# Kernel optimization log

Hardware: AMD Instinct MI355X
Metric: run time of the kernel (lower is better)

## Reference

```python
import jax, jax.numpy as jnp
import numpy as np

CHANNELS = 256
HEADS = 8
HEAD_DIM = CHANNELS // HEADS
SCALE = HEAD_DIM ** (-0.5)


def setup_inputs() -> dict:
    key = jax.random.key(0)
    ks = jax.random.split(key, 9)
    x = jax.random.normal(ks[0], (2, CHANNELS, 64, 64), dtype=jnp.float32)
    # grouped 1x1 conv with groups=heads == per-head [head_dim, head_dim] matmul
    def w(k):
        # kaiming-uniform-ish init scale, faithful enough for a numeric baseline
        bound = 1.0 / np.sqrt(HEAD_DIM)
        return jax.random.uniform(k, (HEADS, HEAD_DIM, HEAD_DIM), dtype=jnp.float32,
                                  minval=-bound, maxval=bound)
    def b(k):
        bound = 1.0 / np.sqrt(HEAD_DIM)
        return jax.random.uniform(k, (HEADS, HEAD_DIM), dtype=jnp.float32,
                                  minval=-bound, maxval=bound)
    return {
        "x": x,
        "Wq": w(ks[1]), "bq": b(ks[2]),
        "Wk": w(ks[3]), "bk": b(ks[4]),
        "Wv": w(ks[5]), "bv": b(ks[6]),
        "Wp": w(ks[7]), "bp": b(ks[8]),
    }


def reference(x, Wq, bq, Wk, bk, Wv, bv, Wp, bp):
    b_, c, h, w = x.shape
    n = h * w
    xh = x.reshape(b_, HEADS, HEAD_DIM, n)  # [b, g, d, n]
    # grouped 1x1 conv == per-head linear over channel dim
    proj = lambda W, bias, t: jnp.einsum('god,bgdn->bgon', W, t) + bias[None, :, :, None]
    q = proj(Wq, bq, xh)  # [b, g, d, n]
    k = proj(Wk, bk, xh)
    v = proj(Wv, bv, xh)
    # attn[b,g,i,j] = sum_d q[b,g,d,i] * k[b,g,d,j] * scale
    attn = jnp.einsum('bgdi,bgdj->bgij', q, k) * SCALE
    attn = jax.nn.softmax(attn, axis=-1)  # [b, g, n, n]
    out = jnp.einsum('bgij,bgdj->bgdi', attn, v)  # [b, g, d, n]
    out = proj(Wp, bp, out)
    return out.reshape(b_, c, h, w)
```

## Files before the change

kernel.cpp:

```cpp
#include <hip/hip_runtime.h>
#include <hip/hip_bf16.h>


constexpr int D = 32;
constexpr int N = 4096;
constexpr int NBG = 16;
constexpr float SCALE = 0.17677669529663687f;
constexpr float LOG2E = 1.4426950408889634f;

using bfrag  = __attribute__((ext_vector_type(8))) short;
using s16x8  = __attribute__((ext_vector_type(8))) short;
using f32x16 = __attribute__((ext_vector_type(16))) float;
typedef unsigned short u16;
typedef unsigned int u32;

constexpr int PSTR = 34;

__device__ __forceinline__ float fexp2(float x) { return __builtin_amdgcn_exp2f(x); }

__device__ __forceinline__ short f2bfs(float f) {
    __hip_bfloat16 h = __float2bfloat16(f);
    return (short)__builtin_bit_cast(u16, h);
}

__device__ __forceinline__ u32 cvt_pk_bf16(float lo, float hi) {
    u32 r;
    asm("v_cvt_pk_bf16_f32 %0, %1, %2" : "=v"(r) : "v"(lo), "v"(hi));
    return r;
}

__global__ __launch_bounds__(256) void proj_kernel(
    const float* __restrict__ x,
    const float* __restrict__ Wq, const float* __restrict__ bq,
    const float* __restrict__ Wk, const float* __restrict__ bk,
    const float* __restrict__ Wv, const float* __restrict__ bv,
    u16* __restrict__ Qb, u16* __restrict__ K2, u16* __restrict__ V2) {
    const int bg = blockIdx.y, g = bg & 7;
    const int z  = blockIdx.z;
    const int i  = blockIdx.x * 256 + threadIdx.x;

    const float* W  = (z == 0) ? Wq : (z == 1) ? Wk : Wv;
    const float* bb = (z == 0) ? bq : (z == 1) ? bk : bv;

    const float* xb = x + (size_t)bg * D * N;
    float xv[D];
#pragma unroll
    for (int d = 0; d < D; ++d) xv[d] = xb[(size_t)d * N + i];

    const float* w = W + g * D * D;
    float acc[D];
#pragma unroll
    for (int o = 0; o < D; ++o) {
        float a0 = 0.f, a1 = 0.f, a2 = 0.f, a3 = 0.f;
#pragma unroll
        for (int d = 0; d < D; d += 4) {
            a0 = fmaf(w[o * D + d    ], xv[d    ], a0);
            a1 = fmaf(w[o * D + d + 1], xv[d + 1], a1);
            a2 = fmaf(w[o * D + d + 2], xv[d + 2], a2);
            a3 = fmaf(w[o * D + d + 3], xv[d + 3], a3);
        }
        acc[o] = (a0 + a1) + (a2 + a3) + bb[g * D + o];
    }

    if (z == 0) {
        u16* dst = Qb + ((size_t)bg * N + i) * D;
#pragma unroll
        for (int t = 0; t < 4; ++t) {
            s16x8 v;
#pragma unroll
            for (int e = 0; e < 8; ++e) v[e] = f2bfs(acc[8 * t + e] * (SCALE * LOG2E));
            *reinterpret_cast<s16x8*>(dst + 8 * t) = v;
        }
    } else if (z == 1) {
        u16* kb2 = K2 + (size_t)bg * N * D;
#pragma unroll
        for (int t = 0; t < 4; ++t) {
            s16x8 v;
#pragma unroll
            for (int e = 0; e < 8; ++e) v[e] = f2bfs(acc[8 * t + e]);
            *reinterpret_cast<s16x8*>(kb2 + (size_t)t * N * 8 + (size_t)i * 8) = v;
        }
    } else {
        const int j  = i & 15;
        const int hh = (j >> 2) & 1;
        const int ee = (j & 3) + 4 * ((j >> 3) & 1);
        u16* vb2 = V2 + (size_t)bg * N * D + (size_t)(i >> 4) * 512 + hh * 256 + ee;
#pragma unroll
        for (int o = 0; o < D; ++o)
            vb2[o * 8] = (u16)f2bfs(acc[o]);
    }
}

__global__ __launch_bounds__(256) void attn_kernel(
    const u16* __restrict__ Qb, const u16* __restrict__ K2, const u16* __restrict__ V2,
    const float* __restrict__ Wp, const float* __restrict__ bp,
    float* __restrict__ out) {
    const int s = blockIdx.x;
    const int bg = s & 15, qt = s >> 4, g = bg & 7;
    const int wid = threadIdx.x >> 6;
    const int lane = threadIdx.x & 63;
    const int l31 = lane & 31, h = lane >> 5;
    const int qbase = qt * 128 + wid * 32;

    __shared__ u16 plds_all[4][32][PSTR];
    u16* tile = &plds_all[wid][0][0];

    const u16* Qw = Qb + (size_t)bg * N * D;
    const u16* Kw = K2 + (size_t)bg * N * D;
    const u16* Vw = V2 + (size_t)bg * N * D;

    const u16* qrow = Qw + (size_t)(qbase + l31) * D + 8 * h;
    bfrag qf0 = *reinterpret_cast<const bfrag*>(qrow);
    bfrag qf1 = *reinterpret_cast<const bfrag*>(qrow + 16);

    bfrag wf0, wf1;
    {
        const float* wrow = Wp + (size_t)(g * D + l31) * D + 8 * h;
#pragma unroll
        for (int e = 0; e < 8; ++e) { wf0[e] = f2bfs(wrow[e]); wf1[e] = f2bfs(wrow[16 + e]); }
    }
    const float bias = bp[g * D + l31];

    bfrag onesf;
#pragma unroll
    for (int e = 0; e < 8; ++e) onesf[e] = (short)0x3F80;

    const f32x16 zf16 = {};
    f32x16 oacc  = {};
    f32x16 lsacc = {};

    const u16* kBase   = Kw + (size_t)h * N * 8 + (size_t)l31 * 8;
    const u16* kHiBase = kBase + 2 * N * 8;
    const u16* vBase   = Vw + h * 256 + l31 * 8;

    const int NT = N / 32;
    const int NP = NT / 2;

    auto ldK  = [&](int tt, int hi) {
        return *reinterpret_cast<const bfrag*>((hi ? kHiBase : kBase) + (size_t)tt * 256);
    };
    auto ldV  = [&](int tt, int half) {
        return *reinterpret_cast<const bfrag*>(vBase + (size_t)tt * 1024 + half * 512);
    };

    bfrag kA0 = ldK(0, 0), kA1 = ldK(0, 1);
    bfrag kB0 = ldK(1, 0), kB1 = ldK(1, 1);
    bfrag vA0 = ldV(0, 0), vA1 = ldV(0, 1);
    bfrag vB0 = ldV(1, 0), vB1 = ldV(1, 1);

    f32x16 sA = __builtin_amdgcn_mfma_f32_32x32x16_bf16(kA0, qf0, zf16, 0, 0, 0);
    sA = __builtin_amdgcn_mfma_f32_32x32x16_bf16(kA1, qf1, sA, 0, 0, 0);
    f32x16 sB = __builtin_amdgcn_mfma_f32_32x32x16_bf16(kB0, qf0, zf16, 0, 0, 0);
    sB = __builtin_amdgcn_mfma_f32_32x32x16_bf16(kB1, qf1, sB, 0, 0, 0);

    kA0 = ldK(2, 0); kA1 = ldK(2, 1);
    kB0 = ldK(3, 0); kB1 = ldK(3, 1);

    for (int t = 0; t < NP - 1; ++t) {
        f32x16 snA = __builtin_amdgcn_mfma_f32_32x32x16_bf16(kA0, qf0, zf16, 0, 0, 0);
        snA = __builtin_amdgcn_mfma_f32_32x32x16_bf16(kA1, qf1, snA, 0, 0, 0);
        f32x16 snB = __builtin_amdgcn_mfma_f32_32x32x16_bf16(kB0, qf0, zf16, 0, 0, 0);
        snB = __builtin_amdgcn_mfma_f32_32x32x16_bf16(kB1, qf1, snB, 0, 0, 0);

        const int t4 = (2 * t + 4 < NT) ? (2 * t + 4) : (NT - 1);
        const int t5 = (2 * t + 5 < NT) ? (2 * t + 5) : (NT - 1);
        kA0 = ldK(t4, 0); kA1 = ldK(t4, 1);
        kB0 = ldK(t5, 0); kB1 = ldK(t5, 1);
        bfrag vnA0 = ldV(2 * t + 2, 0), vnA1 = ldV(2 * t + 2, 1);
        bfrag vnB0 = ldV(2 * t + 3, 0), vnB1 = ldV(2 * t + 3, 1);

        {
            float p[16];
#pragma unroll
            for (int r = 0; r < 16; ++r) p[r] = fexp2(sA[r]);
            uint4 f1 = make_uint4(cvt_pk_bf16(p[0],  p[1]),  cvt_pk_bf16(p[2],  p[3]),
                                  cvt_pk_bf16(p[4],  p[5]),  cvt_pk_bf16(p[6],  p[7]));
            uint4 f2 = make_uint4(cvt_pk_bf16(p[8],  p[9]),  cvt_pk_bf16(p[10], p[11]),
                                  cvt_pk_bf16(p[12], p[13]), cvt_pk_bf16(p[14], p[15]));
            const bfrag pf1 = __builtin_bit_cast(bfrag, f1);
            const bfrag pf2 = __builtin_bit_cast(bfrag, f2);
            oacc  = __builtin_amdgcn_mfma_f32_32x32x16_bf16(pf1, vA0,   oacc,  0, 0, 0);
            oacc  = __builtin_amdgcn_mfma_f32_32x32x16_bf16(pf2, vA1,   oacc,  0, 0, 0);
            lsacc = __builtin_amdgcn_mfma_f32_32x32x16_bf16(pf1, onesf, lsacc, 0, 0, 0);
            lsacc = __builtin_amdgcn_mfma_f32_32x32x16_bf16(pf2, onesf, lsacc, 0, 0, 0);
        }
        {
            float p[16];
#pragma unroll
            for (int r = 0; r < 16; ++r) p[r] = fexp2(sB[r]);
            uint4 f1 = make_uint4(cvt_pk_bf16(p[0],  p[1]),  cvt_pk_bf16(p[2],  p[3]),
                                  cvt_pk_bf16(p[4],  p[5]),  cvt_pk_bf16(p[6],  p[7]));
            uint4 f2 = make_uint4(cvt_pk_bf16(p[8],  p[9]),  cvt_pk_bf16(p[10], p[11]),
                                  cvt_pk_bf16(p[12], p[13]), cvt_pk_bf16(p[14], p[15]));
            const bfrag pf1 = __builtin_bit_cast(bfrag, f1);
            const bfrag pf2 = __builtin_bit_cast(bfrag, f2);
            oacc  = __builtin_amdgcn_mfma_f32_32x32x16_bf16(pf1, vB0,   oacc,  0, 0, 0);
            oacc  = __builtin_amdgcn_mfma_f32_32x32x16_bf16(pf2, vB1,   oacc,  0, 0, 0);
            lsacc = __builtin_amdgcn_mfma_f32_32x32x16_bf16(pf1, onesf, lsacc, 0, 0, 0);
            lsacc = __builtin_amdgcn_mfma_f32_32x32x16_bf16(pf2, onesf, lsacc, 0, 0, 0);
        }

        sA = snA; sB = snB;
        vA0 = vnA0; vA1 = vnA1; vB0 = vnB0; vB1 = vnB1;
    }

#pragma unroll
    for (int c = 0; c < 2; ++c) {
        const f32x16& sc = c ? sB : sA;
        float p[16];
#pragma unroll
        for (int r = 0; r < 16; ++r) p[r] = fexp2(sc[r]);
        uint4 f1 = make_uint4(cvt_pk_bf16(p[0],  p[1]),  cvt_pk_bf16(p[2],  p[3]),
                              cvt_pk_bf16(p[4],  p[5]),  cvt_pk_bf16(p[6],  p[7]));
        uint4 f2 = make_uint4(cvt_pk_bf16(p[8],  p[9]),  cvt_pk_bf16(p[10], p[11]),
                              cvt_pk_bf16(p[12], p[13]), cvt_pk_bf16(p[14], p[15]));
        const bfrag pf1 = __builtin_bit_cast(bfrag, f1);
        const bfrag pf2 = __builtin_bit_cast(bfrag, f2);
        oacc  = __builtin_amdgcn_mfma_f32_32x32x16_bf16(pf1, c ? vB0 : vA0, oacc,  0, 0, 0);
        oacc  = __builtin_amdgcn_mfma_f32_32x32x16_bf16(pf2, c ? vB1 : vA1, oacc,  0, 0, 0);
        lsacc = __builtin_amdgcn_mfma_f32_32x32x16_bf16(pf1, onesf, lsacc, 0, 0, 0);
        lsacc = __builtin_amdgcn_mfma_f32_32x32x16_bf16(pf2, onesf, lsacc, 0, 0, 0);
    }

#pragma unroll
    for (int r = 0; r < 16; ++r) {
        const int q = (r & 3) + 8 * (r >> 2) + 4 * h;
        tile[q * PSTR + l31] = (u16)f2bfs(oacc[r] / lsacc[r]);
    }

    asm volatile("" ::: "memory");

    bfrag oa0 = *reinterpret_cast<const bfrag*>(tile + l31 * PSTR + 8 * h);
    bfrag oa1 = *reinterpret_cast<const bfrag*>(tile + l31 * PSTR + 16 + 8 * h);

    f32x16 oc;
#pragma unroll
    for (int r = 0; r < 16; ++r) oc[r] = bias;
    oc = __builtin_amdgcn_mfma_f32_32x32x16_bf16(oa0, wf0, oc, 0, 0, 0);
    oc = __builtin_amdgcn_mfma_f32_32x32x16_bf16(oa1, wf1, oc, 0, 0, 0);

    float* ob = out + (size_t)(bg * D + l31) * N + qbase + 4 * h;
#pragma unroll
    for (int rr = 0; rr < 4; ++rr)
        *reinterpret_cast<float4*>(ob + 8 * rr) =
            make_float4(oc[4 * rr], oc[4 * rr + 1], oc[4 * rr + 2], oc[4 * rr + 3]);
}

extern "C" void kernel_launch(void* const* d_in, const int* in_sizes, int n_in,
                              void* d_out, int out_size, void* d_ws, size_t ws_size,
                              hipStream_t stream) {
    const float* x  = (const float*)d_in[0];
    const float* Wq = (const float*)d_in[1];
    const float* bq = (const float*)d_in[2];
    const float* Wk = (const float*)d_in[3];
    const float* bk = (const float*)d_in[4];
    const float* Wv = (const float*)d_in[5];
    const float* bv = (const float*)d_in[6];
    const float* Wp = (const float*)d_in[7];
    const float* bp = (const float*)d_in[8];
    float* out = (float*)d_out;

    u16* Qb = (u16*)d_ws;
    u16* K2 = Qb + (size_t)NBG * N * D;
    u16* V2 = K2 + (size_t)NBG * N * D;

    proj_kernel<<<dim3(N / 256, NBG, 3), 256, 0, stream>>>(x, Wq, bq, Wk, bk, Wv, bv, Qb, K2, V2);
    attn_kernel<<<dim3(NBG * (N / 128)), 256, 0, stream>>>(Qb, K2, V2, Wp, bp, out);
}
```

Measured before the change: 70.10 us.

## Split key range across wave pairs and merge partial accumulators in LDS

Each block now covers 64 queries instead of 128. Two waves share each 32-query slice and each processes half of the key/value sequence, so the grid doubles to 1024 blocks. The second wave writes its partial output and row-sum accumulators to shared memory, and after a block barrier the first wave adds them and finishes normalization and the output projection. This shortens each wave's serial loop and raises parallelism, at the cost of extra LDS traffic, a sync, half the waves going idle during the epilogue, and twice the Q/Wp loads overall.

```diff
diff --git a/kernel.cpp b/kernel.cpp
--- a/kernel.cpp
+++ b/kernel.cpp
@@ -98,12 +98,14 @@
     const int s = blockIdx.x;
     const int bg = s & 15, qt = s >> 4, g = bg & 7;
     const int wid = threadIdx.x >> 6;
+    const int qhalf = wid >> 1, khalf = wid & 1;
     const int lane = threadIdx.x & 63;
     const int l31 = lane & 31, h = lane >> 5;
-    const int qbase = qt * 128 + wid * 32;
-
-    __shared__ u16 plds_all[4][32][PSTR];
-    u16* tile = &plds_all[wid][0][0];
+    const int qbase = qt * 64 + qhalf * 32;
+
+    __shared__ float macc[2][32][64];
+    __shared__ u16 plds_all[2][32][PSTR];
+    u16* tile = &plds_all[qhalf][0][0];
 
     const u16* Qw = Qb + (size_t)bg * N * D;
     const u16* Kw = K2 + (size_t)bg * N * D;
@@ -129,17 +131,17 @@
     f32x16 oacc  = {};
     f32x16 lsacc = {};
 
-    const u16* kBase   = Kw + (size_t)h * N * 8 + (size_t)l31 * 8;
+    const u16* kBase   = Kw + (size_t)h * N * 8 + (size_t)l31 * 8 + (size_t)khalf * (N / 2) * 8;
     const u16* kHiBase = kBase + 2 * N * 8;
-    const u16* vBase   = Vw + h * 256 + l31 * 8;
-
-    const int NT = N / 32;
-    const int NP = NT / 2;
-
-    auto ldK  = [&](int tt, int hi) {
+    const u16* vBase   = Vw + h * 256 + l31 * 8 + (size_t)khalf * (N / 2) * 32;
+
+    const int NTL = (N / 2) / 32;
+    const int NPL = NTL / 2;
+
+    auto ldK = [&](int tt, int hi) {
         return *reinterpret_cast<const bfrag*>((hi ? kHiBase : kBase) + (size_t)tt * 256);
     };
-    auto ldV  = [&](int tt, int half) {
+    auto ldV = [&](int tt, int half) {
         return *reinterpret_cast<const bfrag*>(vBase + (size_t)tt * 1024 + half * 512);
     };
 
@@ -156,14 +158,14 @@
     kA0 = ldK(2, 0); kA1 = ldK(2, 1);
     kB0 = ldK(3, 0); kB1 = ldK(3, 1);
 
-    for (int t = 0; t < NP - 1; ++t) {
+    for (int t = 0; t < NPL - 1; ++t) {
         f32x16 snA = __builtin_amdgcn_mfma_f32_32x32x16_bf16(kA0, qf0, zf16, 0, 0, 0);
         snA = __builtin_amdgcn_mfma_f32_32x32x16_bf16(kA1, qf1, snA, 0, 0, 0);
         f32x16 snB = __builtin_amdgcn_mfma_f32_32x32x16_bf16(kB0, qf0, zf16, 0, 0, 0);
         snB = __builtin_amdgcn_mfma_f32_32x32x16_bf16(kB1, qf1, snB, 0, 0, 0);
 
-        const int t4 = (2 * t + 4 < NT) ? (2 * t + 4) : (NT - 1);
-        const int t5 = (2 * t + 5 < NT) ? (2 * t + 5) : (NT - 1);
+        const int t4 = (2 * t + 4 < NTL) ? (2 * t + 4) : (NTL - 1);
+        const int t5 = (2 * t + 5 < NTL) ? (2 * t + 5) : (NTL - 1);
         kA0 = ldK(t4, 0); kA1 = ldK(t4, 1);
         kB0 = ldK(t5, 0); kB1 = ldK(t5, 1);
         bfrag vnA0 = ldV(2 * t + 2, 0), vnA1 = ldV(2 * t + 2, 1);
@@ -221,6 +223,19 @@
         lsacc = __builtin_amdgcn_mfma_f32_32x32x16_bf16(pf1, onesf, lsacc, 0, 0, 0);
         lsacc = __builtin_amdgcn_mfma_f32_32x32x16_bf16(pf2, onesf, lsacc, 0, 0, 0);
     }
+
+    if (khalf == 1) {
+#pragma unroll
+        for (int r = 0; r < 16; ++r) macc[qhalf][r][lane] = oacc[r];
+#pragma unroll
+        for (int r = 0; r < 16; ++r) macc[qhalf][16 + r][lane] = lsacc[r];
+    }
+    __syncthreads();
+    if (khalf == 1) return;
+#pragma unroll
+    for (int r = 0; r < 16; ++r) oacc[r] += macc[qhalf][r][lane];
+#pragma unroll
+    for (int r = 0; r < 16; ++r) lsacc[r] += macc[qhalf][16 + r][lane];
 
 #pragma unroll
     for (int r = 0; r < 16; ++r) {
@@ -265,5 +280,5 @@
     u16* V2 = K2 + (size_t)NBG * N * D;
 
     proj_kernel<<<dim3(N / 256, NBG, 3), 256, 0, stream>>>(x, Wq, bq, Wk, bk, Wv, bv, Qb, K2, V2);
-    attn_kernel<<<dim3(NBG * (N / 128)), 256, 0, stream>>>(Qb, K2, V2, Wp, bp, out);
-}
+    attn_kernel<<<dim3(NBG * (N / 64)), 256, 0, stream>>>(Qb, K2, V2, Wp, bp, out);
+}
```

Result: slower. 72.21 us (median of 2 runs) (+3.0%).
